# Performance work log

Measured on AMD Instinct MI355X. Metric: run time of the kernel, lower is better.

Reference implementation:

```python
import jax, jax.numpy as jnp
import numpy as np

HEADS = 8
DIM_HEAD = 64
EPS = 1e-4


def softmax_kernel(data, proj, is_query):
    # data: [b,h,n,d], proj: [m,d]
    data_normalizer = data.shape[-1] ** -0.25
    ratio = proj.shape[0] ** -0.5
    data_dash = jnp.einsum('bhnd,md->bhnm', data_normalizer * data, proj)
    diag = (data * data).sum(-1) * 0.5 * (data_normalizer ** 2)  # [b,h,n]
    diag = diag[..., None]
    if is_query:
        stab = jnp.max(data_dash, axis=-1, keepdims=True)
    else:
        stab = jnp.max(data_dash)
    return ratio * (jnp.exp(data_dash - diag - stab) + EPS)


def linear_attention(q, k, v):
    # q,k: [b,h,n,m], v: [b,h,n,e]
    k_cumsum = k.sum(axis=-2)  # [b,h,m]
    d_inv = 1.0 / jnp.einsum('bhnm,bhm->bhn', q, k_cumsum)
    context = jnp.einsum('bhnm,bhne->bhme', k, v)  # [b,h,m,e]
    return jnp.einsum('bhme,bhnm,bhn->bhne', context, q, d_inv)


def setup_inputs() -> dict:
    key = jax.random.key(0)
    ks = jax.random.split(key, 6)
    b, n, dim = 8, 4096, 512
    m, dh = 266, DIM_HEAD
    x = jax.random.normal(ks[0], (b, n, dim), dtype=jnp.float32)
    s = dim ** -0.5
    Wq = jax.random.normal(ks[1], (dim, dim), dtype=jnp.float32) * s
    Wk = jax.random.normal(ks[2], (dim, dim), dtype=jnp.float32) * s
    Wv = jax.random.normal(ks[3], (dim, dim), dtype=jnp.float32) * s
    Wo = jax.random.normal(ks[4], (dim, dim), dtype=jnp.float32) * s
    bo = jnp.zeros((dim,), dtype=jnp.float32)
    proj = jax.random.normal(ks[5], (m, dh), dtype=jnp.float32)
    return {"x": x, "Wq": Wq, "Wk": Wk, "Wv": Wv, "Wo": Wo, "bo": bo, "proj": proj}


def reference(x, Wq, Wk, Wv, Wv_unused=None, *, _=None, **__):
    raise NotImplementedError


def reference(x, Wq, Wk, Wv, Wo, bo, proj):
    b, n, dim = x.shape
    h, dh = HEADS, DIM_HEAD
    # Linear projections (weights stored as [in, out])
    q = (x @ Wq).reshape(b, n, h, dh).transpose(0, 2, 1, 3)  # [b,h,n,dh]
    k = (x @ Wk).reshape(b, n, h, dh).transpose(0, 2, 1, 3)
    v = (x @ Wv).reshape(b, n, h, dh).transpose(0, 2, 1, 3)
    qp = softmax_kernel(q, proj, is_query=True)   # [b,h,n,m]
    kp = softmax_kernel(k, proj, is_query=False)  # [b,h,n,m]
    out = linear_attention(qp, kp, v)             # [b,h,n,dh]
    out = out.transpose(0, 2, 1, 3).reshape(b, n, h * dh)
    return out @ Wo + bo
```

## Files before the change

### kernel.cpp

```cpp
#include <hip/hip_runtime.h>
#include <stdint.h>

#define B_ 8
#define N_ 4096
#define H_ 8
#define DH_ 64
#define DIM_ 512
#define M_ 266
#define MP_ 320
#define BH_ 64
#define BNROWS_ 32768
#define NS_ 8
#define CN_ 0.35355339059327373f
#define RATIO_ 0.06131393394849658f
#define EPS_ 1e-4f
#define REPS_ (RATIO_ * EPS_)

typedef __bf16 bf16x8 __attribute__((ext_vector_type(8)));
typedef float f32x4 __attribute__((ext_vector_type(4)));

union U8 { bf16x8 v; uint4 u; uint2 u2[2]; uint16_t s[8]; };

__device__ __forceinline__ uint32_t f2bf(float f) {
  uint32_t u = __float_as_uint(f);
  u += 0x7FFFu + ((u >> 16) & 1u);
  return u >> 16;
}
__device__ __forceinline__ uint32_t pkbf(float a, float b) {
  uint32_t r;
  asm("v_cvt_pk_bf16_f32 %0, %1, %2" : "=v"(r) : "v"(a), "v"(b));
  return r;
}
__device__ __forceinline__ float bflo(uint32_t u) { return __uint_as_float(u << 16); }
__device__ __forceinline__ float bfhi(uint32_t u) { return __uint_as_float(u & 0xFFFF0000u); }
__device__ __forceinline__ void unp8(uint4 u, float* f) {
  f[0] = bflo(u.x); f[1] = bfhi(u.x); f[2] = bflo(u.y); f[3] = bfhi(u.y);
  f[4] = bflo(u.z); f[5] = bfhi(u.z); f[6] = bflo(u.w); f[7] = bfhi(u.w);
}
__device__ __forceinline__ float f4get(const float4& v, int i) {
  return ((const float*)&v)[i];
}
__device__ __forceinline__ uint32_t fenc(float f) {
  uint32_t u = __float_as_uint(f);
  return u ^ ((uint32_t)((int32_t)u >> 31) | 0x80000000u);
}
__device__ __forceinline__ float fdec(uint32_t e) {
  uint32_t u = (e & 0x80000000u) ? (e ^ 0x80000000u) : ~e;
  return __uint_as_float(u);
}
__device__ __forceinline__ int piperm(int p) {
  int tmt = p >> 4, r = p & 15;
  return 32 * (tmt >> 1) + 8 * (r >> 2) + 4 * (tmt & 1) + (r & 3);
}
__device__ __forceinline__ int phinv(int r) {
  int lo = r & 15;
  return 8 * (lo >> 2) + (lo & 3) + ((r >> 4) << 2);
}
__device__ __forceinline__ void glds16(const uint16_t* g, uint16_t* l) {
  __builtin_amdgcn_global_load_lds(
      (const __attribute__((address_space(1))) void*)g,
      (__attribute__((address_space(3))) void*)l, 16, 0, 0);
}

__global__ void init_stab(uint32_t* s) { *s = fenc(-3.4e38f); }

__global__ __launch_bounds__(256) void cast_x(const float* __restrict__ x,
                                              uint16_t* __restrict__ xb, int n4) {
  for (int i = blockIdx.x * 256 + threadIdx.x; i < n4; i += 2048 * 256) {
    float4 v = ((const float4*)x)[i];
    uint2 o;
    o.x = f2bf(v.x) | (f2bf(v.y) << 16);
    o.y = f2bf(v.z) | (f2bf(v.w) << 16);
    ((uint2*)xb)[i] = o;
  }
}

__global__ __launch_bounds__(256) void cast_weights(const float* __restrict__ Wq,
                                                    const float* __restrict__ Wk,
                                                    const float* __restrict__ Wv,
                                                    const float* __restrict__ Wo,
                                                    const float* __restrict__ proj,
                                                    uint16_t* __restrict__ wqkvT,
                                                    uint16_t* __restrict__ woT,
                                                    uint16_t* __restrict__ projb) {
  int idx = blockIdx.x * 256 + threadIdx.x;
  if (idx < 4 * 262144) {
    int which = idx >> 18, i = idx & 262143;
    const float* src = which == 0 ? Wq : which == 1 ? Wk : which == 2 ? Wv : Wo;
    uint16_t* dst = which < 3 ? wqkvT + (size_t)which * 262144 : woT;
    int k = i >> 9, n = i & 511;
    dst[(size_t)n * 512 + k] = (uint16_t)f2bf(src[i]);
  } else {
    int i = idx - 4 * 262144;
    if (i < MP_ * DH_) {
      int p = i >> 6, d = i & 63;
      int pi = piperm(p);
      float v = (pi < M_) ? proj[pi * DH_ + d] : 0.f;
      projb[i] = (uint16_t)f2bf(v);
    }
  }
}

template <int EPI, int NBY>
__global__ __launch_bounds__(256) void gemm_glds(const uint16_t* __restrict__ A,
                                                 const uint16_t* __restrict__ Bt,
                                                 float* __restrict__ outF,
                                                 const float* __restrict__ bias,
                                                 uint16_t* __restrict__ qb,
                                                 uint16_t* __restrict__ kbuf,
                                                 uint16_t* __restrict__ vTb) {
  __shared__ __align__(16) uint16_t smem[17408];
  uint16_t (*AsArr)[4096] = (uint16_t (*)[4096])smem;
  uint16_t (*BsArr)[4096] = (uint16_t (*)[4096])(smem + 8192);
  uint16_t (*epi)[136] = (uint16_t (*)[136])smem;
  const int t = threadIdx.x, lane = t & 63, w = t >> 6;
  const int g = lane >> 4, r16 = lane & 15;
  const int wr = (w >> 1) * 64, wc = (w & 1) * 64;
  const int flat = blockIdx.x;
  const int xcd = flat & 7, jj = flat >> 3;
  const int bxoff = jj / NBY, by = jj - bxoff * NBY;
  const int bx = xcd * 32 + bxoff;
  const size_t rowA0 = (size_t)bx * 128;
  const size_t rowB0 = (size_t)by * 128;
  const int K = 512;

  f32x4 acc[4][4];
#pragma unroll
  for (int i = 0; i < 4; ++i)
#pragma unroll
    for (int j = 0; j < 4; ++j) acc[i][j] = (f32x4){0.f, 0.f, 0.f, 0.f};

  auto stageG = [&](int kt, int buf) {
#pragma unroll
    for (int s = 0; s < 2; ++s) {
      const int row = w * 32 + s * 16;
      const uint16_t* ga = A + (rowA0 + row + (lane >> 2)) * (size_t)K + kt * 32 + (lane & 3) * 8;
      glds16(ga, &AsArr[buf][row * 32]);
      const uint16_t* gb = Bt + (rowB0 + row + (lane >> 2)) * (size_t)K + kt * 32 + (lane & 3) * 8;
      glds16(gb, &BsArr[buf][row * 32]);
    }
  };
  stageG(0, 0);
  for (int kt = 0; kt < 16; ++kt) {
    __syncthreads();
    if (kt + 1 < 16) stageG(kt + 1, (kt + 1) & 1);
    const uint16_t* as = AsArr[kt & 1];
    const uint16_t* bs = BsArr[kt & 1];
    bf16x8 af[4], bfr[4];
#pragma unroll
    for (int i = 0; i < 4; ++i)
      af[i] = *(const bf16x8*)&as[(wr + i * 16 + r16) * 32 + g * 8];
#pragma unroll
    for (int j = 0; j < 4; ++j)
      bfr[j] = *(const bf16x8*)&bs[(wc + j * 16 + r16) * 32 + g * 8];
#pragma unroll
    for (int i = 0; i < 4; ++i)
#pragma unroll
      for (int j = 0; j < 4; ++j)
        acc[i][j] = __builtin_amdgcn_mfma_f32_16x16x32_bf16(af[i], bfr[j], acc[i][j], 0, 0, 0);
  }
  if constexpr (EPI == 0) {
#pragma unroll
    for (int i = 0; i < 4; ++i) {
      const size_t row0 = rowA0 + wr + i * 16 + g * 4;
#pragma unroll
      for (int j = 0; j < 4; ++j) {
        const size_t col = rowB0 + wc + j * 16 + r16;
        float badd = bias ? bias[col] : 0.f;
#pragma unroll
        for (int q = 0; q < 4; ++q)
          outF[(row0 + q) * (size_t)512 + col] = acc[i][j][q] + badd;
      }
    }
  } else {
    const int region = by >> 2;
    const int lcolBase = (by & 3) * 128;
    __syncthreads();
    if (region <= 1) {
#pragma unroll
      for (int i = 0; i < 4; ++i)
#pragma unroll
        for (int j = 0; j < 4; ++j)
#pragma unroll
          for (int q = 0; q < 4; ++q)
            epi[wr + i * 16 + g * 4 + q][wc + j * 16 + r16] = (uint16_t)f2bf(acc[i][j][q]);
    } else {
#pragma unroll
      for (int i = 0; i < 4; ++i)
#pragma unroll
        for (int j = 0; j < 4; ++j)
#pragma unroll
          for (int q = 0; q < 4; ++q)
            epi[wc + j * 16 + r16][wr + i * 16 + g * 4 + q] = (uint16_t)f2bf(acc[i][j][q]);
    }
    __syncthreads();
    const int srow = t >> 4, scol = (t & 15) * 8;
    if (region <= 1) {
      uint16_t* dst = region ? kbuf : qb;
#pragma unroll
      for (int pass = 0; pass < 8; ++pass) {
        const int row = pass * 16 + srow;
        uint4 v = *(const uint4*)&epi[row][scol];
        *(uint4*)&dst[(rowA0 + row) * (size_t)512 + lcolBase + scol] = v;
      }
    } else {
      const int bb = (int)(rowA0 >> 12), nmod = (int)(rowA0 & 4095);
#pragma unroll
      for (int pass = 0; pass < 8; ++pass) {
        const int erow = pass * 16 + srow;
        const int lcol = lcolBase + erow;
        const int hh = lcol >> 6, e = lcol & 63;
        uint4 v = *(const uint4*)&epi[erow][scol];
        *(uint4*)&vTb[((size_t)((bb * 8 + hh) * 64 + e)) * 4096 + nmod + scol] = v;
      }
    }
  }
}

__global__ __launch_bounds__(256) void stab2_mfma(const uint16_t* __restrict__ kb,
                                                  const uint16_t* __restrict__ projb,
                                                  uint32_t* __restrict__ stab) {
  __shared__ uint16_t kt[2][32][72];
  __shared__ float wred[4];
  const int t = threadIdx.x, lane = t & 63, w = t >> 6;
  const int g = lane >> 4, r16 = lane & 15;
  const int bh = blockIdx.x, ns = blockIdx.y;
  const int b = bh >> 3, h = bh & 7;
  bf16x8 pj[5][2];
  bool mval[5];
#pragma unroll
  for (int mt = 0; mt < 5; ++mt) {
    int m16 = mt * 64 + w * 16;
    pj[mt][0] = *(const bf16x8*)&projb[(m16 + r16) * 64 + g * 8];
    pj[mt][1] = *(const bf16x8*)&projb[(m16 + r16) * 64 + 32 + g * 8];
    mval[mt] = piperm(m16 + r16) < M_;
  }
  auto stage = [&](int it, int buf) {
    int n0 = ns * 128 + it * 32;
    int row = t >> 3, c8 = t & 7;
    *(uint4*)&kt[buf][row][c8 * 8] =
        *(const uint4*)&kb[((size_t)(b * N_ + n0 + row)) * DIM_ + h * DH_ + c8 * 8];
  };
  stage(0, 0);
  __syncthreads();
  float vmax = -3.4e38f;
  for (int it = 0; it < 4; ++it) {
    int cur = it & 1;
    if (it + 1 < 4) stage(it + 1, cur ^ 1);
    bf16x8 ka[2][2];
#pragma unroll
    for (int nsub = 0; nsub < 2; ++nsub) {
      ka[nsub][0] = *(const bf16x8*)&kt[cur][nsub * 16 + r16][g * 8];
      ka[nsub][1] = *(const bf16x8*)&kt[cur][nsub * 16 + r16][32 + g * 8];
    }
#pragma unroll
    for (int mt = 0; mt < 5; ++mt) {
#pragma unroll
      for (int nsub = 0; nsub < 2; ++nsub) {
        f32x4 c4 = (f32x4){0.f, 0.f, 0.f, 0.f};
        c4 = __builtin_amdgcn_mfma_f32_16x16x32_bf16(ka[nsub][0], pj[mt][0], c4, 0, 0, 0);
        c4 = __builtin_amdgcn_mfma_f32_16x16x32_bf16(ka[nsub][1], pj[mt][1], c4, 0, 0, 0);
        if (mval[mt])
          vmax = fmaxf(vmax, fmaxf(fmaxf(c4[0], c4[1]), fmaxf(c4[2], c4[3])));
      }
    }
    __syncthreads();
  }
#pragma unroll
  for (int off = 32; off; off >>= 1) vmax = fmaxf(vmax, __shfl_xor(vmax, off));
  if (lane == 0) wred[w] = vmax;
  __syncthreads();
  if (t == 0) {
    float m = fmaxf(fmaxf(wred[0], wred[1]), fmaxf(wred[2], wred[3]));
    atomicMax(stab, fenc(CN_ * m));
  }
}

__global__ __launch_bounds__(256) void ctx_mfma(const uint16_t* __restrict__ kb,
                                                const uint16_t* __restrict__ vTb,
                                                const uint16_t* __restrict__ projb,
                                                const uint32_t* __restrict__ stab_e,
                                                uint16_t* __restrict__ ctxpb,
                                                float* __restrict__ kcump) {
  __shared__ uint16_t kt[2][32][72];
  __shared__ uint16_t vt[2][64][40];
  __shared__ float dk2[2][32];
  __shared__ uint16_t kpb[4][16][40];
  const int t = threadIdx.x, lane = t & 63, w = t >> 6;
  const int g = lane >> 4, r16 = lane & 15;
  const int id = blockIdx.x;
  const int xcd = id & 7, j5 = id >> 3;
  const int mt = j5 % 5, pair = j5 / 5;
  const int bhns = xcd * 64 + pair;
  const int bh = bhns >> 3, ns = bhns & 7;
  const int b = bh >> 3, h = bh & 7;
  const int m16 = mt * 64 + w * 16;
  const float stab = fdec(*stab_e);
  const bool mvalid = piperm(m16 + r16) < M_;
  bf16x8 pj0 = *(const bf16x8*)&projb[(m16 + r16) * 64 + g * 8];
  bf16x8 pj1 = *(const bf16x8*)&projb[(m16 + r16) * 64 + 32 + g * 8];
  const int iters = 4096 / (32 * NS_);

  auto stage = [&](int it, int buf) {
    int n0 = (ns * iters + it) * 32;
    {
      int row = t >> 3, c8 = t & 7;
      uint4 kv = *(const uint4*)&kb[((size_t)(b * N_ + n0 + row)) * DIM_ + h * DH_ + c8 * 8];
      *(uint4*)&kt[buf][row][c8 * 8] = kv;
      float f[8]; unp8(kv, f);
      float sq = f[0]*f[0]+f[1]*f[1]+f[2]*f[2]+f[3]*f[3]+f[4]*f[4]+f[5]*f[5]+f[6]*f[6]+f[7]*f[7];
      sq += __shfl_xor(sq, 1); sq += __shfl_xor(sq, 2); sq += __shfl_xor(sq, 4);
      if (c8 == 0) dk2[buf][row] = 0.5f * CN_ * CN_ * sq;
    }
    {
      int e = t >> 2, c = t & 3;
      uint4 vv = *(const uint4*)&vTb[((size_t)(bh * 64 + e)) * 4096 + n0 + c * 8];
      *(uint4*)&vt[buf][e][c * 8] = vv;
    }
  };
  f32x4 acc[4];
#pragma unroll
  for (int j = 0; j < 4; ++j) acc[j] = (f32x4){0.f, 0.f, 0.f, 0.f};
  float kcacc = 0.f;

  stage(0, 0);
  __syncthreads();
  for (int it = 0; it < iters; ++it) {
    int cur = it & 1;
    if (it + 1 < iters) stage(it + 1, cur ^ 1);
#pragma unroll
    for (int nsub = 0; nsub < 2; ++nsub) {
      bf16x8 ka0 = *(const bf16x8*)&kt[cur][nsub * 16 + r16][g * 8];
      bf16x8 ka1 = *(const bf16x8*)&kt[cur][nsub * 16 + r16][32 + g * 8];
      f32x4 c4 = (f32x4){0.f, 0.f, 0.f, 0.f};
      c4 = __builtin_amdgcn_mfma_f32_16x16x32_bf16(ka0, pj0, c4, 0, 0, 0);
      c4 = __builtin_amdgcn_mfma_f32_16x16x32_bf16(ka1, pj1, c4, 0, 0, 0);
      float4 dkv = *(const float4*)&dk2[cur][nsub * 16 + 4 * g];
      float kp[4];
#pragma unroll
      for (int q = 0; q < 4; ++q) {
        float arg = CN_ * c4[q] - f4get(dkv, q) - stab;
        float e = RATIO_ * __expf(arg) + REPS_;
        kp[q] = mvalid ? e : 0.f;
        kcacc += kp[q];
      }
      *(uint2*)&kpb[w][r16][nsub * 16 + 4 * g] = make_uint2(pkbf(kp[0], kp[1]), pkbf(kp[2], kp[3]));
    }
    U8 kq; kq.u = *(const uint4*)&kpb[w][r16][g * 8];
#pragma unroll
    for (int j = 0; j < 4; ++j) {
      U8 vf; vf.u = *(const uint4*)&vt[cur][j * 16 + r16][g * 8];
      acc[j] = __builtin_amdgcn_mfma_f32_16x16x32_bf16(kq.v, vf.v, acc[j], 0, 0, 0);
    }
    __syncthreads();
  }
#pragma unroll
  for (int j = 0; j < 4; ++j) {
    uint2 o;
    o.x = pkbf(acc[j][0], acc[j][1]);
    o.y = pkbf(acc[j][2], acc[j][3]);
    *(uint2*)&ctxpb[(((size_t)ns * BH_ + bh) * 64 + j * 16 + r16) * MP_ + m16 + 4 * g] = o;
  }
  kcacc += __shfl_xor(kcacc, 16);
  kcacc += __shfl_xor(kcacc, 32);
  if (lane < 16) kcump[((size_t)ns * BH_ + bh) * MP_ + m16 + lane] = kcacc;
}

__global__ __launch_bounds__(256) void merge_kernel(const uint16_t* __restrict__ ctxpb,
                                                    const float* __restrict__ kcump,
                                                    uint16_t* __restrict__ ctxgb,
                                                    float* __restrict__ kcumg) {
  int idx = blockIdx.x * 256 + threadIdx.x;
  const int total = BH_ * 64 * MP_;
  if (idx < total) {
    float s = 0.f;
#pragma unroll
    for (int p = 0; p < NS_; ++p)
      s += __uint_as_float((uint32_t)ctxpb[(size_t)p * total + idx] << 16);
    int row = idx / MP_;
    int pos = idx - row * MP_;
    int col = (pos & ~31) + phinv(pos & 31);
    ctxgb[(size_t)row * MP_ + col] = (uint16_t)f2bf(s);
  }
  const int ktotal = BH_ * MP_;
  if (idx < ktotal) {
    float s = 0.f;
#pragma unroll
    for (int p = 0; p < NS_; ++p) s += kcump[(size_t)p * ktotal + idx];
    kcumg[idx] = s;
  }
}

__global__ __launch_bounds__(512) void attn_mfma(const uint16_t* __restrict__ qb,
                                                 const uint16_t* __restrict__ projb,
                                                 const uint16_t* __restrict__ ctxgb,
                                                 const float* __restrict__ kcumg,
                                                 uint16_t* __restrict__ attnb) {
  __shared__ uint16_t ctile[64][328];
  __shared__ uint16_t qs[128][72];
  __shared__ float kcums[MP_];
  __shared__ float dqs[128];
  __shared__ float denb[8][16];
  const int t = threadIdx.x, lane = t & 63, w = t >> 6;
  const int g = lane >> 4, r16 = lane & 15;
  const int nch = blockIdx.x, bh = blockIdx.y;
  const int b = bh >> 3, h = bh & 7;
  {
    int row = t >> 3, cb = t & 7;
#pragma unroll
    for (int cc = 0; cc < 5; ++cc) {
      int cN = cb * 40 + cc * 8;
      *(uint4*)&ctile[row][cN] = *(const uint4*)&ctxgb[((size_t)bh * 64 + row) * MP_ + cN];
    }
  }
  if (t < MP_) kcums[t] = kcumg[(size_t)bh * MP_ + t];

  for (int it = 0; it < 4; ++it) {
    const int nbase = nch * 512 + it * 128;
    __syncthreads();
    {
      int row = t >> 2, c2 = t & 3;
      float sq = 0.f;
#pragma unroll
      for (int cc = 0; cc < 2; ++cc) {
        int c8 = c2 * 2 + cc;
        uint4 qv = *(const uint4*)&qb[((size_t)(b * N_ + nbase + row)) * DIM_ + h * DH_ + c8 * 8];
        *(uint4*)&qs[row][c8 * 8] = qv;
        float f[8]; unp8(qv, f);
        sq += f[0]*f[0]+f[1]*f[1]+f[2]*f[2]+f[3]*f[3]+f[4]*f[4]+f[5]*f[5]+f[6]*f[6]+f[7]*f[7];
      }
      sq += __shfl_xor(sq, 1); sq += __shfl_xor(sq, 2);
      if (c2 == 0) dqs[row] = 0.5f * CN_ * CN_ * sq;
    }
    __syncthreads();
    bf16x8 qf0 = *(const bf16x8*)&qs[w * 16 + r16][g * 8];
    bf16x8 qf1 = *(const bf16x8*)&qs[w * 16 + r16][32 + g * 8];
    f32x4 S[18];
#pragma unroll
    for (int mt = 0; mt < 18; ++mt) {
      bf16x8 pa0 = *(const bf16x8*)&projb[(mt * 16 + r16) * 64 + g * 8];
      bf16x8 pa1 = *(const bf16x8*)&projb[(mt * 16 + r16) * 64 + 32 + g * 8];
      f32x4 c4 = (f32x4){0.f, 0.f, 0.f, 0.f};
      c4 = __builtin_amdgcn_mfma_f32_16x16x32_bf16(pa0, qf0, c4, 0, 0, 0);
      S[mt] = __builtin_amdgcn_mfma_f32_16x16x32_bf16(pa1, qf1, c4, 0, 0, 0);
    }
    float rmax = -3.4e38f;
#pragma unroll
    for (int mt = 0; mt < 18; ++mt) {
#pragma unroll
      for (int q = 0; q < 4; ++q) {
        bool val = (mt < 16) || (256 + 4 * (mt & 1) + 8 * g + q < M_);
        if (val) rmax = fmaxf(rmax, CN_ * S[mt][q]);
      }
    }
    rmax = fmaxf(rmax, __shfl_xor(rmax, 16));
    rmax = fmaxf(rmax, __shfl_xor(rmax, 32));
    const float offv = rmax + dqs[w * 16 + r16];
    float denp = 0.f;
    uint32_t pk[18][2];
#pragma unroll
    for (int mt = 0; mt < 18; ++mt) {
      float4 kc4 = *(const float4*)&kcums[mt * 16 + 4 * g];
      float qp[4];
#pragma unroll
      for (int q = 0; q < 4; ++q) {
        bool val = (mt < 16) || (256 + 4 * (mt & 1) + 8 * g + q < M_);
        float e = RATIO_ * __expf(CN_ * S[mt][q] - offv) + REPS_;
        qp[q] = val ? e : 0.f;
        denp += qp[q] * f4get(kc4, q);
      }
      pk[mt][0] = pkbf(qp[0], qp[1]);
      pk[mt][1] = pkbf(qp[2], qp[3]);
    }
    denp += __shfl_xor(denp, 16);
    denp += __shfl_xor(denp, 32);
    if (lane < 16) denb[w][lane] = denp;
    f32x4 o[4];
#pragma unroll
    for (int j = 0; j < 4; ++j) o[j] = (f32x4){0.f, 0.f, 0.f, 0.f};
#pragma unroll
    for (int s = 0; s < 9; ++s) {
      U8 af; af.u = make_uint4(pk[2 * s][0], pk[2 * s][1], pk[2 * s + 1][0], pk[2 * s + 1][1]);
#pragma unroll
      for (int j = 0; j < 4; ++j) {
        U8 cf; cf.u = *(const uint4*)&ctile[j * 16 + r16][s * 32 + g * 8];
        o[j] = __builtin_amdgcn_mfma_f32_16x16x32_bf16(af.v, cf.v, o[j], 0, 0, 0);
      }
    }
    float4 dv = *(const float4*)&denb[w][4 * g];
    float rd[4];
#pragma unroll
    for (int q = 0; q < 4; ++q) rd[q] = 1.0f / f4get(dv, q);
    __syncthreads();
#pragma unroll
    for (int j = 0; j < 4; ++j)
#pragma unroll
      for (int q = 0; q < 4; ++q)
        qs[w * 16 + 4 * g + q][j * 16 + r16] = (uint16_t)f2bf(o[j][q] * rd[q]);
    __syncthreads();
    {
      const int srow = t >> 3, scol = (t & 7) * 8;
#pragma unroll
      for (int pass = 0; pass < 2; ++pass) {
        const int row = pass * 64 + srow;
        uint4 v = *(const uint4*)&qs[row][scol];
        *(uint4*)&attnb[((size_t)(b * N_ + nbase + row)) * DIM_ + h * DH_ + scol] = v;
      }
    }
  }
}

extern "C" void kernel_launch(void* const* d_in, const int* in_sizes, int n_in,
                              void* d_out, int out_size, void* d_ws, size_t ws_size,
                              hipStream_t stream) {
  const float* x = (const float*)d_in[0];
  const float* Wq = (const float*)d_in[1];
  const float* Wk = (const float*)d_in[2];
  const float* Wv = (const float*)d_in[3];
  const float* Wo = (const float*)d_in[4];
  const float* bo = (const float*)d_in[5];
  const float* proj = (const float*)d_in[6];
  float* out = (float*)d_out;

  char* ws = (char*)d_ws;
  size_t off = 0;
  auto alloc = [&](size_t bytes) {
    char* p = ws + off;
    off += (bytes + 255) & ~(size_t)255;
    return p;
  };
  uint16_t* wqkvT = (uint16_t*)alloc((size_t)1536 * 512 * 2);
  uint16_t* woT = (uint16_t*)alloc((size_t)512 * 512 * 2);
  uint16_t* projb = (uint16_t*)alloc((size_t)MP_ * DH_ * 2);
  uint16_t* vTb = (uint16_t*)alloc((size_t)BNROWS_ * DIM_ * 2);
  uint16_t* ctxpb = (uint16_t*)alloc((size_t)NS_ * BH_ * 64 * MP_ * 2);
  float* kcump = (float*)alloc((size_t)NS_ * BH_ * MP_ * 4);
  uint16_t* ctxgb = (uint16_t*)alloc((size_t)BH_ * 64 * MP_ * 2);
  float* kcumg = (float*)alloc((size_t)BH_ * MP_ * 4);
  uint32_t* stab = (uint32_t*)alloc(256);
  uint16_t* xb = (uint16_t*)alloc((size_t)BNROWS_ * DIM_ * 2);
  uint16_t* qb = (uint16_t*)d_out;
  uint16_t* kb = qb + (size_t)BNROWS_ * DIM_;
  uint16_t* attnb = vTb;

  init_stab<<<1, 1, 0, stream>>>(stab);
  cast_weights<<<4176, 256, 0, stream>>>(Wq, Wk, Wv, Wo, proj, wqkvT, woT, projb);
  cast_x<<<2048, 256, 0, stream>>>(x, xb, BNROWS_ * DIM_ / 4);

  gemm_glds<1, 12><<<3072, 256, 0, stream>>>(xb, wqkvT, nullptr, nullptr, qb, kb, vTb);

  stab2_mfma<<<dim3(64, 32), 256, 0, stream>>>(kb, projb, stab);
  ctx_mfma<<<2560, 256, 0, stream>>>(kb, vTb, projb, stab, ctxpb, kcump);
  merge_kernel<<<5120, 256, 0, stream>>>(ctxpb, kcump, ctxgb, kcumg);
  attn_mfma<<<dim3(8, 64), 512, 0, stream>>>(qb, projb, ctxgb, kcumg, attnb);
  gemm_glds<0, 4><<<1024, 256, 0, stream>>>(attnb, woT, out, bo, nullptr, nullptr, nullptr);
}
```

Measured before the change: 272.7 us.

## Widen GEMM tiles to 128x256 with 512 threads, fold stab init, split attn grid

```diff
diff --git a/kernel.cpp b/kernel.cpp
--- a/kernel.cpp
+++ b/kernel.cpp
@@ -62,8 +62,6 @@
       (__attribute__((address_space(3))) void*)l, 16, 0, 0);
 }
 
-__global__ void init_stab(uint32_t* s) { *s = fenc(-3.4e38f); }
-
 __global__ __launch_bounds__(256) void cast_x(const float* __restrict__ x,
                                               uint16_t* __restrict__ xb, int n4) {
   for (int i = blockIdx.x * 256 + threadIdx.x; i < n4; i += 2048 * 256) {
@@ -82,7 +80,8 @@
                                                     const float* __restrict__ proj,
                                                     uint16_t* __restrict__ wqkvT,
                                                     uint16_t* __restrict__ woT,
-                                                    uint16_t* __restrict__ projb) {
+                                                    uint16_t* __restrict__ projb,
+                                                    uint32_t* __restrict__ stab) {
   int idx = blockIdx.x * 256 + threadIdx.x;
   if (idx < 4 * 262144) {
     int which = idx >> 18, i = idx & 262143;
@@ -97,31 +96,33 @@
       int pi = piperm(p);
       float v = (pi < M_) ? proj[pi * DH_ + d] : 0.f;
       projb[i] = (uint16_t)f2bf(v);
+    } else if (i == MP_ * DH_) {
+      *stab = fenc(-3.4e38f);
     }
   }
 }
 
 template <int EPI, int NBY>
-__global__ __launch_bounds__(256) void gemm_glds(const uint16_t* __restrict__ A,
+__global__ __launch_bounds__(512) void gemm_glds(const uint16_t* __restrict__ A,
                                                  const uint16_t* __restrict__ Bt,
                                                  float* __restrict__ outF,
                                                  const float* __restrict__ bias,
                                                  uint16_t* __restrict__ qb,
                                                  uint16_t* __restrict__ kbuf,
                                                  uint16_t* __restrict__ vTb) {
-  __shared__ __align__(16) uint16_t smem[17408];
+  __shared__ __align__(16) uint16_t smem[24576];
   uint16_t (*AsArr)[4096] = (uint16_t (*)[4096])smem;
-  uint16_t (*BsArr)[4096] = (uint16_t (*)[4096])(smem + 8192);
+  uint16_t (*BsArr)[8192] = (uint16_t (*)[8192])(smem + 8192);
   uint16_t (*epi)[136] = (uint16_t (*)[136])smem;
   const int t = threadIdx.x, lane = t & 63, w = t >> 6;
   const int g = lane >> 4, r16 = lane & 15;
-  const int wr = (w >> 1) * 64, wc = (w & 1) * 64;
+  const int wr = (w >> 2) * 64, wc = (w & 3) * 64;
   const int flat = blockIdx.x;
   const int xcd = flat & 7, jj = flat >> 3;
   const int bxoff = jj / NBY, by = jj - bxoff * NBY;
   const int bx = xcd * 32 + bxoff;
   const size_t rowA0 = (size_t)bx * 128;
-  const size_t rowB0 = (size_t)by * 128;
+  const size_t rowB0 = (size_t)by * 256;
   const int K = 512;
 
   f32x4 acc[4][4];
@@ -131,11 +132,11 @@
     for (int j = 0; j < 4; ++j) acc[i][j] = (f32x4){0.f, 0.f, 0.f, 0.f};
 
   auto stageG = [&](int kt, int buf) {
+    const uint16_t* ga = A + (rowA0 + w * 16 + (lane >> 2)) * (size_t)K + kt * 32 + (lane & 3) * 8;
+    glds16(ga, &AsArr[buf][(w * 16) * 32]);
 #pragma unroll
     for (int s = 0; s < 2; ++s) {
       const int row = w * 32 + s * 16;
-      const uint16_t* ga = A + (rowA0 + row + (lane >> 2)) * (size_t)K + kt * 32 + (lane & 3) * 8;
-      glds16(ga, &AsArr[buf][row * 32]);
       const uint16_t* gb = Bt + (rowB0 + row + (lane >> 2)) * (size_t)K + kt * 32 + (lane & 3) * 8;
       glds16(gb, &BsArr[buf][row * 32]);
     }
@@ -173,46 +174,53 @@
       }
     }
   } else {
-    const int region = by >> 2;
-    const int lcolBase = (by & 3) * 128;
-    __syncthreads();
-    if (region <= 1) {
-#pragma unroll
-      for (int i = 0; i < 4; ++i)
-#pragma unroll
-        for (int j = 0; j < 4; ++j)
-#pragma unroll
-          for (int q = 0; q < 4; ++q)
-            epi[wr + i * 16 + g * 4 + q][wc + j * 16 + r16] = (uint16_t)f2bf(acc[i][j][q]);
-    } else {
-#pragma unroll
-      for (int i = 0; i < 4; ++i)
-#pragma unroll
-        for (int j = 0; j < 4; ++j)
-#pragma unroll
-          for (int q = 0; q < 4; ++q)
-            epi[wc + j * 16 + r16][wr + i * 16 + g * 4 + q] = (uint16_t)f2bf(acc[i][j][q]);
-    }
-    __syncthreads();
-    const int srow = t >> 4, scol = (t & 15) * 8;
-    if (region <= 1) {
-      uint16_t* dst = region ? kbuf : qb;
-#pragma unroll
-      for (int pass = 0; pass < 8; ++pass) {
-        const int row = pass * 16 + srow;
-        uint4 v = *(const uint4*)&epi[row][scol];
-        *(uint4*)&dst[(rowA0 + row) * (size_t)512 + lcolBase + scol] = v;
-      }
-    } else {
-      const int bb = (int)(rowA0 >> 12), nmod = (int)(rowA0 & 4095);
-#pragma unroll
-      for (int pass = 0; pass < 8; ++pass) {
-        const int erow = pass * 16 + srow;
-        const int lcol = lcolBase + erow;
-        const int hh = lcol >> 6, e = lcol & 63;
-        uint4 v = *(const uint4*)&epi[erow][scol];
-        *(uint4*)&vTb[((size_t)((bb * 8 + hh) * 64 + e)) * 4096 + nmod + scol] = v;
-      }
+    const int region = by >> 1;
+    const int lcol512base = (by & 1) * 256;
+    __syncthreads();
+#pragma unroll
+    for (int ch = 0; ch < 2; ++ch) {
+      if (((w & 3) >> 1) == ch) {
+        const int wcl = ((w & 3) & 1) * 64;
+        if (region <= 1) {
+#pragma unroll
+          for (int i = 0; i < 4; ++i)
+#pragma unroll
+            for (int j = 0; j < 4; ++j)
+#pragma unroll
+              for (int q = 0; q < 4; ++q)
+                epi[wr + i * 16 + g * 4 + q][wcl + j * 16 + r16] = (uint16_t)f2bf(acc[i][j][q]);
+        } else {
+#pragma unroll
+          for (int i = 0; i < 4; ++i)
+#pragma unroll
+            for (int j = 0; j < 4; ++j)
+#pragma unroll
+              for (int q = 0; q < 4; ++q)
+                epi[wcl + j * 16 + r16][wr + i * 16 + g * 4 + q] = (uint16_t)f2bf(acc[i][j][q]);
+        }
+      }
+      __syncthreads();
+      const int srow = t >> 4, scol = (t & 15) * 8;
+      if (region <= 1) {
+        uint16_t* dst = region ? kbuf : qb;
+#pragma unroll
+        for (int pass = 0; pass < 4; ++pass) {
+          const int row = pass * 32 + srow;
+          uint4 v = *(const uint4*)&epi[row][scol];
+          *(uint4*)&dst[(rowA0 + row) * (size_t)512 + lcol512base + ch * 128 + scol] = v;
+        }
+      } else {
+        const int bb = (int)(rowA0 >> 12), nmod = (int)(rowA0 & 4095);
+#pragma unroll
+        for (int pass = 0; pass < 4; ++pass) {
+          const int erow = pass * 32 + srow;
+          const int lcol512 = lcol512base + ch * 128 + erow;
+          const int hh = lcol512 >> 6, e = lcol512 & 63;
+          uint4 v = *(const uint4*)&epi[erow][scol];
+          *(uint4*)&vTb[((size_t)((bb * 8 + hh) * 64 + e)) * 4096 + nmod + scol] = v;
+        }
+      }
+      __syncthreads();
     }
   }
 }
@@ -415,8 +423,8 @@
   }
   if (t < MP_) kcums[t] = kcumg[(size_t)bh * MP_ + t];
 
-  for (int it = 0; it < 4; ++it) {
-    const int nbase = nch * 512 + it * 128;
+  for (int it = 0; it < 2; ++it) {
+    const int nbase = nch * 256 + it * 128;
     __syncthreads();
     {
       int row = t >> 2, c2 = t & 3;
@@ -543,15 +551,14 @@
   uint16_t* kb = qb + (size_t)BNROWS_ * DIM_;
   uint16_t* attnb = vTb;
 
-  init_stab<<<1, 1, 0, stream>>>(stab);
-  cast_weights<<<4176, 256, 0, stream>>>(Wq, Wk, Wv, Wo, proj, wqkvT, woT, projb);
+  cast_weights<<<4177, 256, 0, stream>>>(Wq, Wk, Wv, Wo, proj, wqkvT, woT, projb, stab);
   cast_x<<<2048, 256, 0, stream>>>(x, xb, BNROWS_ * DIM_ / 4);
 
-  gemm_glds<1, 12><<<3072, 256, 0, stream>>>(xb, wqkvT, nullptr, nullptr, qb, kb, vTb);
+  gemm_glds<1, 6><<<1536, 512, 0, stream>>>(xb, wqkvT, nullptr, nullptr, qb, kb, vTb);
 
   stab2_mfma<<<dim3(64, 32), 256, 0, stream>>>(kb, projb, stab);
   ctx_mfma<<<2560, 256, 0, stream>>>(kb, vTb, projb, stab, ctxpb, kcump);
   merge_kernel<<<5120, 256, 0, stream>>>(ctxpb, kcump, ctxgb, kcumg);
-  attn_mfma<<<dim3(8, 64), 512, 0, stream>>>(qb, projb, ctxgb, kcumg, attnb);
-  gemm_glds<0, 4><<<1024, 256, 0, stream>>>(attnb, woT, out, bo, nullptr, nullptr, nullptr);
-}
+  attn_mfma<<<dim3(16, 64), 512, 0, stream>>>(qb, projb, ctxgb, kcumg, attnb);
+  gemm_glds<0, 2><<<512, 512, 0, stream>>>(attnb, woT, out, bo, nullptr, nullptr, nullptr);
+}
```

Result: slower. 295.8 us (+8.5%).
